# Performance work log

Measured on AMD Instinct MI355X. Metric: run time of the kernel, lower is better.

The kernel has to match this reference:

```python
import jax, jax.numpy as jnp
import numpy as np

W_DIM = 72  # positional_encoding(3 coords, 12 freqs) -> 3*12*2
_F1 = np.array([1.0, 3.0, 3.0, 1.0], dtype=np.float32)
_F2 = np.outer(_F1, _F1); _F2 = _F2 / _F2.sum()  # normalized StyleGAN resample filter


def upsample2x(x):
    """Antialiased 2x upsample: zero-insertion + 4-tap [1,3,3,1] FIR, gain=4 (upfirdn2d)."""
    C = x.shape[1]
    k = jnp.tile(jnp.asarray(_F2 * 4.0, x.dtype)[None, None], (C, 1, 1, 1))  # [C,1,4,4]
    return jax.lax.conv_general_dilated(
        x, k, (1, 1), ((2, 2), (2, 2)), lhs_dilation=(2, 2),
        feature_group_count=C, dimension_numbers=('NCHW', 'OIHW', 'NCHW'))


def affine(w_vec, aw, ab):
    # FullyConnectedLayer: runtime weight gain 1/sqrt(w_dim), bias init 1
    return (w_vec @ aw.T) / np.sqrt(W_DIM) + ab


def mod_conv(x, weight, styles, demodulate=True, padding=1):
    """StyleGAN2 modulated conv2d (batch=1). weight [Co,Ci,k,k], styles [Ci]."""
    w = weight * styles[None, :, None, None]
    if demodulate:
        d = jax.lax.rsqrt(jnp.sum(w * w, axis=(1, 2, 3)) + 1e-8)
        w = w * d[:, None, None, None]
    return jax.lax.conv_general_dilated(
        x, w, (1, 1), ((padding, padding), (padding, padding)),
        dimension_numbers=('NCHW', 'OIHW', 'NCHW'))


def syn_layer(x, w_vec, aw, ab, cw, cb, up):
    s = affine(w_vec, aw, ab)
    if up:
        x = upsample2x(x)
    x = mod_conv(x, cw, s, True, 1)
    # bias_act: lrelu, gain sqrt(2), conv_clamp 256 (noise_strength init 0 -> no noise)
    x = jax.nn.leaky_relu(x + cb[None, :, None, None], 0.2) * np.sqrt(2.0)
    return jnp.clip(x, -256.0, 256.0)


def to_rgb(x, w_vec, aw, ab, cw, cb):
    s = affine(w_vec, aw, ab) / np.sqrt(cw.shape[1])  # ToRGB weight_gain 1/sqrt(Cin)
    y = mod_conv(x, cw, s, False, 0)
    return jnp.clip(y + cb[None, :, None, None], -256.0, 256.0)


def reference(rays, rgbs, conv_w, conv_b, bn_gamma, bn_beta, bn_mean, bn_var,
              a0_w, a0_b, w0, b0, a1_w, a1_b, w1, b1, t0_aw, t0_ab, t0_w, t0_b,
              a2_w, a2_b, w2, b2, a3_w, a3_b, w3, b3, t1_aw, t1_ab, t1_w, t1_b):
    # style vector from positional encoding of ray origin
    p = rays[0, :3, 0, 0]
    fb = 2.0 ** jnp.arange(12, dtype=rays.dtype)
    pts = (p[:, None] * fb[None, :]).reshape(-1)  # (36,)
    w_vec = jnp.concatenate([jnp.sin(pts), jnp.cos(pts)])  # (72,)
    # mapping: 1x1 conv + relu + BatchNorm2d (eval-mode)
    feat = jnp.einsum('oi,bihw->bohw', conv_w[:, :, 0, 0], rgbs) + conv_b[None, :, None, None]
    feat = jax.nn.relu(feat)
    inv = jax.lax.rsqrt(bn_var + 1e-5)
    feat = (feat - bn_mean[None, :, None, None]) * (inv * bn_gamma)[None, :, None, None] + bn_beta[None, :, None, None]
    rgb = feat[:, :3]
    # block0: 32ch@128 -> 256ch@256, skip-architecture ToRGB
    x = syn_layer(feat, w_vec, a0_w, a0_b, w0, b0, True)
    x = syn_layer(x, w_vec, a1_w, a1_b, w1, b1, False)
    img = upsample2x(rgb) + to_rgb(x, w_vec, t0_aw, t0_ab, t0_w, t0_b)
    # block1: 256ch@256 -> 128ch@512
    x = syn_layer(x, w_vec, a2_w, a2_b, w2, b2, True)
    x = syn_layer(x, w_vec, a3_w, a3_b, w3, b3, False)
    img = upsample2x(img) + to_rgb(x, w_vec, t1_aw, t1_ab, t1_w, t1_b)
    return img  # [1,3,512,512]


def setup_inputs() -> dict:
    key = jax.random.key(0)
    ks = jax.random.split(key, 16)
    rn = lambda k, s: jax.random.normal(k, s, dtype=jnp.float32)
    z = lambda s: jnp.zeros(s, jnp.float32)
    o = lambda s: jnp.ones(s, jnp.float32)
    inp = {}
    inp['rays'] = rn(ks[0], (1, 6, 128, 128))
    inp['rgbs'] = jax.random.uniform(ks[1], (1, 3, 128, 128), dtype=jnp.float32)
    inp['conv_w'] = rn(ks[2], (32, 3, 1, 1)); inp['conv_b'] = z((32,))
    inp['bn_gamma'] = o((32,)); inp['bn_beta'] = z((32,))
    inp['bn_mean'] = z((32,)); inp['bn_var'] = o((32,))
    inp['a0_w'] = rn(ks[3], (32, 72)); inp['a0_b'] = o((32,))
    inp['w0'] = rn(ks[4], (256, 32, 3, 3)); inp['b0'] = z((256,))
    inp['a1_w'] = rn(ks[5], (256, 72)); inp['a1_b'] = o((256,))
    inp['w1'] = rn(ks[6], (256, 256, 3, 3)); inp['b1'] = z((256,))
    inp['t0_aw'] = rn(ks[7], (256, 72)); inp['t0_ab'] = o((256,))
    inp['t0_w'] = rn(ks[8], (3, 256, 1, 1)); inp['t0_b'] = z((3,))
    inp['a2_w'] = rn(ks[9], (256, 72)); inp['a2_b'] = o((256,))
    inp['w2'] = rn(ks[10], (128, 256, 3, 3)); inp['b2'] = z((128,))
    inp['a3_w'] = rn(ks[11], (128, 72)); inp['a3_b'] = o((128,))
    inp['w3'] = rn(ks[12], (128, 128, 3, 3)); inp['b3'] = z((128,))
    inp['t1_aw'] = rn(ks[13], (128, 72)); inp['t1_ab'] = o((128,))
    inp['t1_w'] = rn(ks[14], (3, 128, 1, 1)); inp['t1_b'] = z((3,))
    return inp
```

## Files before the change

kernel.cpp:

```cpp
#include <hip/hip_runtime.h>
#include <cstddef>

typedef __attribute__((ext_vector_type(8))) short short8;
typedef __attribute__((ext_vector_type(4))) float f32x4;
typedef __attribute__((address_space(3))) void lds_void;
typedef const __attribute__((address_space(1))) void glob_void;

static const size_t OFF_S0    = 0;
static const size_t OFF_S1    = 64;
static const size_t OFF_S2    = 320;
static const size_t OFF_S3    = 576;
static const size_t OFF_MT0   = 704;
static const size_t OFF_MT1   = 1472;
static const size_t OFF_ZERO  = 1856;
static const size_t OFF_RGBF  = 2048;
static const size_t OFF_IMG0  = 51200;
static const size_t OFF_RGBP  = 247808;
static const size_t OFF_WQ0   = 1900544;
static const size_t OFF_WQ1   = 1937408;
static const size_t OFF_WQ2   = 2232320;
static const size_t OFF_WQ3   = 2379776;
static const size_t OFF_FEAT  = 2453504;
static const size_t OFF_UFEAT = 2715648;
static const size_t OFF_X1    = 4194304;
static const size_t OFF_X2    = 4194304;
static const size_t OFF_U     = 20971520;
static const size_t OFF_X0    = 20971520;

__device__ __forceinline__ unsigned short f2bf(float f) {
  unsigned int u = __float_as_uint(f);
  return (unsigned short)((u + 0x7FFFu + ((u >> 16) & 1u)) >> 16);
}
__device__ __forceinline__ float b2f(short h) {
  return __uint_as_float(((unsigned int)(unsigned short)h) << 16);
}

__global__ void __launch_bounds__(256) prep_kernel(
    const float* __restrict__ rays,
    const float* __restrict__ a0w, const float* __restrict__ a0b,
    const float* __restrict__ a1w, const float* __restrict__ a1b,
    const float* __restrict__ t0aw, const float* __restrict__ t0ab,
    const float* __restrict__ a2w, const float* __restrict__ a2b,
    const float* __restrict__ a3w, const float* __restrict__ a3b,
    const float* __restrict__ t1aw, const float* __restrict__ t1ab,
    const float* __restrict__ t0w, const float* __restrict__ t1w,
    float* __restrict__ ws)
{
  __shared__ float wv[72];
  __shared__ float st0l[256];
  __shared__ float st1l[128];
  const int tid = threadIdx.x;
  if (tid < 128) ws[OFF_ZERO + tid] = 0.f;
  if (tid < 36) {
    int i = tid / 12, j = tid % 12;
    float v = rays[i * 16384] * (float)(1 << j);
    wv[tid]      = sinf(v);
    wv[36 + tid] = cosf(v);
  }
  __syncthreads();
  const float inv72 = 0.11785113019775793f;

  if (tid < 32) {
    float d = 0.f;
    for (int k = 0; k < 72; ++k) d += wv[k] * a0w[tid * 72 + k];
    ws[OFF_S0 + tid] = fmaf(d, inv72, a0b[tid]);
  }
  {
    float d = 0.f;
    for (int k = 0; k < 72; ++k) d += wv[k] * a1w[tid * 72 + k];
    ws[OFF_S1 + tid] = fmaf(d, inv72, a1b[tid]);
  }
  {
    float d = 0.f;
    for (int k = 0; k < 72; ++k) d += wv[k] * t0aw[tid * 72 + k];
    st0l[tid] = fmaf(d, inv72, t0ab[tid]) * 0.0625f;
  }
  {
    float d = 0.f;
    for (int k = 0; k < 72; ++k) d += wv[k] * a2w[tid * 72 + k];
    ws[OFF_S2 + tid] = fmaf(d, inv72, a2b[tid]);
  }
  if (tid < 128) {
    float d = 0.f;
    for (int k = 0; k < 72; ++k) d += wv[k] * a3w[tid * 72 + k];
    ws[OFF_S3 + tid] = fmaf(d, inv72, a3b[tid]);
  }
  if (tid < 128) {
    float d = 0.f;
    for (int k = 0; k < 72; ++k) d += wv[k] * t1aw[tid * 72 + k];
    st1l[tid] = fmaf(d, inv72, t1ab[tid]) * 0.08838834764831845f;
  }
  __syncthreads();
  for (int i = tid; i < 768; i += 256) ws[OFF_MT0 + i] = t0w[i] * st0l[i & 255];
  for (int i = tid; i < 384; i += 256) ws[OFF_MT1 + i] = t1w[i] * st1l[i & 127];
}

__global__ void __launch_bounds__(256) modw_kernel(
    const float* __restrict__ w, const float* __restrict__ s,
    unsigned short* __restrict__ wq, int Ci, int Co)
{
  const int co = blockIdx.x;
  const int n = Ci * 9;
  float local = 0.f;
  for (int i = threadIdx.x; i < n; i += 256) {
    float v = w[co * n + i] * s[i / 9];
    local += v * v;
  }
#pragma unroll
  for (int off = 32; off >= 1; off >>= 1) local += __shfl_xor(local, off);
  __shared__ float red[4];
  if ((threadIdx.x & 63) == 0) red[threadIdx.x >> 6] = local;
  __syncthreads();
  const float d = rsqrtf(red[0] + red[1] + red[2] + red[3] + 1e-8f);
  const int sxor = (co & 3) ^ ((co >> 2) & 3);
  for (int i = threadIdx.x; i < n; i += 256) {
    int ci = i / 9, t = i - ci * 9;
    int kk = ci & 31;
    int sl = (kk >> 3) ^ sxor;
    wq[(((size_t)(ci >> 5) * 9 + t) * Co + co) * 32 + (sl << 3) + (kk & 7)] =
        f2bf(w[co * n + i] * s[ci] * d);
  }
}

__global__ void __launch_bounds__(256) feat_kernel(
    const float* __restrict__ rgbs, const float* __restrict__ cw, const float* __restrict__ cb,
    const float* __restrict__ gam, const float* __restrict__ bet,
    const float* __restrict__ mean, const float* __restrict__ var,
    unsigned short* __restrict__ feat, float* __restrict__ rgbf)
{
  const int p = blockIdx.x * 256 + threadIdx.x;
  const float r = rgbs[p], g = rgbs[16384 + p], b = rgbs[32768 + p];
  unsigned int pk[16];
#pragma unroll
  for (int co = 0; co < 32; ++co) {
    float v = cw[co * 3] * r + cw[co * 3 + 1] * g + cw[co * 3 + 2] * b + cb[co];
    v = fmaxf(v, 0.f);
    float inv = rsqrtf(var[co] + 1e-5f);
    v = (v - mean[co]) * (inv * gam[co]) + bet[co];
    if (co < 3) rgbf[co * 16384 + p] = v;
    unsigned int h = f2bf(v);
    if ((co & 1) == 0) pk[co >> 1] = h;
    else               pk[co >> 1] |= h << 16;
  }
  uint4* dst = reinterpret_cast<uint4*>(feat + (size_t)p * 32);
#pragma unroll
  for (int q = 0; q < 4; ++q)
    dst[q] = make_uint4(pk[q * 4], pk[q * 4 + 1], pk[q * 4 + 2], pk[q * 4 + 3]);
}

__global__ void __launch_bounds__(256) up2x_nhwc_kernel(
    const unsigned short* __restrict__ in, unsigned short* __restrict__ out,
    int H, int W, int c8s , int w2s )
{
  const int cid = blockIdx.x * 256 + threadIdx.x;
  const int k = cid & ((1 << c8s) - 1);
  const int pix = cid >> c8s;
  const int ey = pix >> w2s;
  const int ex = pix & ((1 << w2s) - 1);
  const int C = 8 << c8s;
  int ry0; float ay0, ay1;
  if (ey & 1) { ry0 = ey >> 1;       ay0 = 0.75f; ay1 = 0.25f; }
  else        { ry0 = (ey >> 1) - 1; ay0 = 0.25f; ay1 = 0.75f; }
  int cx0; float bx0, bx1;
  if (ex & 1) { cx0 = ex >> 1;       bx0 = 0.75f; bx1 = 0.25f; }
  else        { cx0 = (ex >> 1) - 1; bx0 = 0.25f; bx1 = 0.75f; }
  const short8 z = {0, 0, 0, 0, 0, 0, 0, 0};
  short8 v00 = z, v01 = z, v10 = z, v11 = z;
  const bool yo0 = (ry0 >= 0), yo1 = (ry0 + 1 < H);
  const bool xo0 = (cx0 >= 0), xo1 = (cx0 + 1 < W);
  if (yo0 && xo0) v00 = *reinterpret_cast<const short8*>(in + ((size_t)(ry0 * W + cx0) * C + k * 8));
  if (yo0 && xo1) v01 = *reinterpret_cast<const short8*>(in + ((size_t)(ry0 * W + cx0 + 1) * C + k * 8));
  if (yo1 && xo0) v10 = *reinterpret_cast<const short8*>(in + ((size_t)((ry0 + 1) * W + cx0) * C + k * 8));
  if (yo1 && xo1) v11 = *reinterpret_cast<const short8*>(in + ((size_t)((ry0 + 1) * W + cx0 + 1) * C + k * 8));
  unsigned int o[4];
#pragma unroll
  for (int j = 0; j < 8; ++j) {
    float f = ay0 * (bx0 * b2f(v00[j]) + bx1 * b2f(v01[j]))
            + ay1 * (bx0 * b2f(v10[j]) + bx1 * b2f(v11[j]));
    unsigned int h = f2bf(f);
    if ((j & 1) == 0) o[j >> 1] = h;
    else              o[j >> 1] |= h << 16;
  }
  *reinterpret_cast<uint4*>(out + (size_t)pix * C + k * 8) = make_uint4(o[0], o[1], o[2], o[3]);
}

template <bool FUSE_RGB>
__global__ void __launch_bounds__(512) conv3x3_mfma(
    const unsigned short* __restrict__ in,
    const unsigned short* __restrict__ wq,
    const float* __restrict__ bias,
    unsigned short* __restrict__ out,
    const float* __restrict__ rgbw,
    float* __restrict__ rgbp,
    const unsigned short* __restrict__ zpage,
    int H, int W, int Ci, int Co)
{
  const int tid  = threadIdx.x;
  const int lane = tid & 63;
  const int wv   = tid >> 6;
  const int wr   = wv & 3;
  const int wg   = wv >> 2;
  const int lo   = lane & 15, hi = lane >> 4;
  const int tpr  = W >> 4;
  const int T_y  = (blockIdx.x / tpr) << 4;
  const int T_x  = (blockIdx.x % tpr) << 4;
  const int cogB = blockIdx.y << 7;
  const int cog  = cogB + (wg << 6);

  __shared__ short8 xs[2][1296];
  __shared__ short8 wlds[2][1536];
  __shared__ float  rw[FUSE_RGB ? 384 : 4];

  if (FUSE_RGB) {
    for (int i = tid; i < 3 * Co; i += 512) rw[i] = rgbw[i];
  }

  f32x4 acc[4][4];
#pragma unroll
  for (int a = 0; a < 4; ++a)
#pragma unroll
    for (int b = 0; b < 4; ++b) acc[a][b] = (f32x4){0.f, 0.f, 0.f, 0.f};

  const unsigned short* gsrc[3];
#pragma unroll
  for (int j = 0; j < 3; ++j) {
    const int s = j * 512 + tid;
    const int pix = s >> 2, kslot = s & 3;
    const int rr = pix / 18, cc = pix - rr * 18;
    const int gy = T_y - 1 + rr, gx = T_x - 1 + cc;
    const int k = kslot ^ ((cc >> 1) & 3);
    const bool inb = (s < 1296) && gy >= 0 && gy < H && gx >= 0 && gx < W;
    gsrc[j] = inb ? (in + ((size_t)(gy * W + gx) * Ci + (k << 3))) : zpage;
  }

#define STAGE(c, buf)                                                              \
  {                                                                                \
    const int cb_ = (c) << 5;                                                      \
    _Pragma("unroll")                                                              \
    for (int j = 0; j < 2; ++j)                                                    \
      __builtin_amdgcn_global_load_lds((glob_void*)(gsrc[j] + cb_),                \
                                       (lds_void*)&xs[buf][j * 512 + tid], 16, 0, 0); \
    if (tid < 272)                                                                 \
      __builtin_amdgcn_global_load_lds((glob_void*)(gsrc[2] + cb_),                \
                                       (lds_void*)&xs[buf][1024 + tid], 16, 0, 0); \
  }

#define STAGE_W(C, KX, BUF)                                                        \
  {                                                                                \
    _Pragma("unroll")                                                              \
    for (int j = 0; j < 3; ++j) {                                                  \
      const unsigned short* src_ =                                                 \
          wq + ((size_t)((C) * 9 + j * 3 + (KX)) * Co + cogB) * 32 + tid * 8;      \
      __builtin_amdgcn_global_load_lds((glob_void*)src_,                           \
                                       (lds_void*)&wlds[BUF][(j << 9) + tid], 16, 0, 0); \
    }                                                                              \
  }

  const int sxa   = (lo & 3) ^ ((lo >> 2) & 3);
  const int wbase = (((wg << 6) + lo) << 2) + (hi ^ sxa);
#define ALOADW(SLOT, KY, BUF)                                                      \
  {                                                                                \
    _Pragma("unroll")                                                              \
    for (int cf = 0; cf < 4; ++cf)                                                 \
      apf[SLOT][cf] = wlds[BUF][((KY) << 9) + wbase + (cf << 6)];                  \
  }

  STAGE(0, 0);
  STAGE_W(0, 0, 0);
  __syncthreads();

  const int nch = Ci >> 5;
  const int rstride = 72;
  int wb = 0;
  for (int c = 0; c < nch; ++c) {
    const int cur = c & 1;
#pragma unroll
    for (int g = 0; g < 3; ++g) {
      if (g < 2)             { STAGE_W(c, g + 1, wb ^ 1); }
      else if (c + 1 < nch)  { STAGE_W(c + 1, 0, wb ^ 1); }
      if (g == 0 && c + 1 < nch) STAGE(c + 1, cur ^ 1);

      const int tx2  = lo + g;
      const int xv_  = hi ^ ((tx2 >> 1) & 3);
      const int rowb = (((wr << 2) * 18 + tx2) << 2) + xv_;
      short8 b0 = xs[cur][rowb];
      short8 b1 = xs[cur][rowb + rstride];
      short8 b2 = xs[cur][rowb + 2 * rstride];
      short8 b3 = xs[cur][rowb + 3 * rstride];

      short8 apf[2][4];
      ALOADW(0, 0, wb);
      ALOADW(1, 1, wb);
#pragma unroll
      for (int cf = 0; cf < 4; ++cf) {
        acc[cf][0] = __builtin_amdgcn_mfma_f32_16x16x32_bf16(apf[0][cf], b0, acc[cf][0], 0, 0, 0);
        acc[cf][1] = __builtin_amdgcn_mfma_f32_16x16x32_bf16(apf[0][cf], b1, acc[cf][1], 0, 0, 0);
        acc[cf][2] = __builtin_amdgcn_mfma_f32_16x16x32_bf16(apf[0][cf], b2, acc[cf][2], 0, 0, 0);
        acc[cf][3] = __builtin_amdgcn_mfma_f32_16x16x32_bf16(apf[0][cf], b3, acc[cf][3], 0, 0, 0);
      }
      b0 = xs[cur][rowb + 4 * rstride];
      ALOADW(0, 2, wb);
#pragma unroll
      for (int cf = 0; cf < 4; ++cf) {
        acc[cf][0] = __builtin_amdgcn_mfma_f32_16x16x32_bf16(apf[1][cf], b1, acc[cf][0], 0, 0, 0);
        acc[cf][1] = __builtin_amdgcn_mfma_f32_16x16x32_bf16(apf[1][cf], b2, acc[cf][1], 0, 0, 0);
        acc[cf][2] = __builtin_amdgcn_mfma_f32_16x16x32_bf16(apf[1][cf], b3, acc[cf][2], 0, 0, 0);
        acc[cf][3] = __builtin_amdgcn_mfma_f32_16x16x32_bf16(apf[1][cf], b0, acc[cf][3], 0, 0, 0);
      }
      b1 = xs[cur][rowb + 5 * rstride];
#pragma unroll
      for (int cf = 0; cf < 4; ++cf) {
        acc[cf][0] = __builtin_amdgcn_mfma_f32_16x16x32_bf16(apf[0][cf], b2, acc[cf][0], 0, 0, 0);
        acc[cf][1] = __builtin_amdgcn_mfma_f32_16x16x32_bf16(apf[0][cf], b3, acc[cf][1], 0, 0, 0);
        acc[cf][2] = __builtin_amdgcn_mfma_f32_16x16x32_bf16(apf[0][cf], b0, acc[cf][2], 0, 0, 0);
        acc[cf][3] = __builtin_amdgcn_mfma_f32_16x16x32_bf16(apf[0][cf], b1, acc[cf][3], 0, 0, 0);
      }
      __syncthreads();
      wb ^= 1;
    }
  }
#undef STAGE
#undef STAGE_W
#undef ALOADW

  const float rt2 = 1.41421356237309515f;
#pragma unroll
  for (int r = 0; r < 4; ++r) {
    const int gy = T_y + (wr << 2) + r;
    const int gx = T_x + lo;
    if (!FUSE_RGB) {
#pragma unroll
      for (int cf = 0; cf < 4; ++cf) {
        const int cb = cog + (cf << 4) + (hi << 2);
        const f32x4 bi = *reinterpret_cast<const f32x4*>(bias + cb);
        unsigned short h[4];
#pragma unroll
        for (int reg = 0; reg < 4; ++reg) {
          float vv = acc[cf][r][reg] + bi[reg];
          vv = (vv >= 0.f) ? vv : 0.2f * vv;
          vv *= rt2;
          vv = fminf(fmaxf(vv, -256.f), 256.f);
          h[reg] = f2bf(vv);
        }
        uint2 pk;
        pk.x = (unsigned int)h[0] | ((unsigned int)h[1] << 16);
        pk.y = (unsigned int)h[2] | ((unsigned int)h[3] << 16);
        *reinterpret_cast<uint2*>(out + (size_t)(gy * W + gx) * Co + cb) = pk;
      }
    } else {
      float p0 = 0.f, p1 = 0.f, p2 = 0.f;
#pragma unroll
      for (int cf = 0; cf < 4; ++cf) {
        const int cb = cog + (cf << 4) + (hi << 2);
        const f32x4 bi = *reinterpret_cast<const f32x4*>(bias + cb);
#pragma unroll
        for (int reg = 0; reg < 4; ++reg) {
          float vv = acc[cf][r][reg] + bi[reg];
          vv = (vv >= 0.f) ? vv : 0.2f * vv;
          vv *= rt2;
          vv = fminf(fmaxf(vv, -256.f), 256.f);
          p0 = fmaf(rw[cb + reg], vv, p0);
          p1 = fmaf(rw[Co + cb + reg], vv, p1);
          p2 = fmaf(rw[2 * Co + cb + reg], vv, p2);
        }
      }
      p0 += __shfl_xor(p0, 16); p0 += __shfl_xor(p0, 32);
      p1 += __shfl_xor(p1, 16); p1 += __shfl_xor(p1, 32);
      p2 += __shfl_xor(p2, 16); p2 += __shfl_xor(p2, 32);
      if (hi == 0) {
        const size_t HWs = (size_t)H * W;
        const size_t px  = (size_t)gy * W + gx;
        rgbp[((size_t)wg * 3 + 0) * HWs + px] = p0;
        rgbp[((size_t)wg * 3 + 1) * HWs + px] = p1;
        rgbp[((size_t)wg * 3 + 2) * HWs + px] = p2;
      }
    }
  }
}

__device__ __forceinline__ float up2x_sample(const float* __restrict__ im, int H, int W,
                                             int oy, int ox)
{
  int my = oy >> 1, mx = ox >> 1;
  int ry0; float ay0, ay1;
  if (oy & 1) { ry0 = my;     ay0 = 0.75f; ay1 = 0.25f; }
  else        { ry0 = my - 1; ay0 = 0.25f; ay1 = 0.75f; }
  int cx0; float bx0, bx1;
  if (ox & 1) { cx0 = mx;     bx0 = 0.75f; bx1 = 0.25f; }
  else        { cx0 = mx - 1; bx0 = 0.25f; bx1 = 0.75f; }
  float v00 = (ry0 >= 0    && cx0 >= 0   ) ? im[ry0 * W + cx0]           : 0.f;
  float v01 = (ry0 >= 0    && cx0 + 1 < W) ? im[ry0 * W + cx0 + 1]       : 0.f;
  float v10 = (ry0 + 1 < H && cx0 >= 0   ) ? im[(ry0 + 1) * W + cx0]     : 0.f;
  float v11 = (ry0 + 1 < H && cx0 + 1 < W) ? im[(ry0 + 1) * W + cx0 + 1] : 0.f;
  return ay0 * (bx0 * v00 + bx1 * v01) + ay1 * (bx0 * v10 + bx1 * v11);
}

__global__ void __launch_bounds__(256) img0_kernel(
    const float* __restrict__ rgbf, const unsigned short* __restrict__ x1,
    const float* __restrict__ mt0g, const float* __restrict__ tb,
    float* __restrict__ img0)
{
  __shared__ float mt[768];
  const int tid = threadIdx.x;
  for (int i = tid; i < 768; i += 256) mt[i] = mt0g[i];
  __syncthreads();
  const int p = blockIdx.x * 256 + tid;
  const unsigned short* xp = x1 + (size_t)p * 256;
  float a0 = 0.f, a1 = 0.f, a2 = 0.f;
  for (int i8 = 0; i8 < 32; ++i8) {
    const short8 v = *reinterpret_cast<const short8*>(xp + i8 * 8);
#pragma unroll
    for (int j = 0; j < 8; ++j) {
      const float xv = b2f(v[j]);
      const int ci = i8 * 8 + j;
      a0 = fmaf(mt[ci],       xv, a0);
      a1 = fmaf(mt[256 + ci], xv, a1);
      a2 = fmaf(mt[512 + ci], xv, a2);
    }
  }
  const int oy = p >> 8, ox = p & 255;
  float av[3] = {a0, a1, a2};
#pragma unroll
  for (int o = 0; o < 3; ++o) {
    float y = fminf(fmaxf(av[o] + tb[o], -256.f), 256.f);
    img0[o * 65536 + p] = up2x_sample(rgbf + o * 16384, 128, 128, oy, ox) + y;
  }
}

__global__ void __launch_bounds__(256) final_kernel(
    const float* __restrict__ img0, const float* __restrict__ rgbp,
    const float* __restrict__ tb, float* __restrict__ out)
{
  const int p = blockIdx.x * 256 + threadIdx.x;
  const int oy = p >> 9, ox = p & 511;
#pragma unroll
  for (int o = 0; o < 3; ++o) {
    float a = rgbp[(0 * 3 + o) * 262144 + p] + rgbp[(1 * 3 + o) * 262144 + p];
    float y = fminf(fmaxf(a + tb[o], -256.f), 256.f);
    out[o * 262144 + p] = up2x_sample(img0 + o * 65536, 256, 256, oy, ox) + y;
  }
}

extern "C" void kernel_launch(void* const* d_in, const int* in_sizes, int n_in,
                              void* d_out, int out_size, void* d_ws, size_t ws_size,
                              hipStream_t stream)
{
  const float* rays   = (const float*)d_in[0];
  const float* rgbs   = (const float*)d_in[1];
  const float* conv_w = (const float*)d_in[2];
  const float* conv_b = (const float*)d_in[3];
  const float* bn_g   = (const float*)d_in[4];
  const float* bn_b   = (const float*)d_in[5];
  const float* bn_m   = (const float*)d_in[6];
  const float* bn_v   = (const float*)d_in[7];
  const float* a0_w   = (const float*)d_in[8];
  const float* a0_b   = (const float*)d_in[9];
  const float* w0     = (const float*)d_in[10];
  const float* b0     = (const float*)d_in[11];
  const float* a1_w   = (const float*)d_in[12];
  const float* a1_b   = (const float*)d_in[13];
  const float* w1     = (const float*)d_in[14];
  const float* b1     = (const float*)d_in[15];
  const float* t0_aw  = (const float*)d_in[16];
  const float* t0_ab  = (const float*)d_in[17];
  const float* t0_w   = (const float*)d_in[18];
  const float* t0_b   = (const float*)d_in[19];
  const float* a2_w   = (const float*)d_in[20];
  const float* a2_b   = (const float*)d_in[21];
  const float* w2     = (const float*)d_in[22];
  const float* b2     = (const float*)d_in[23];
  const float* a3_w   = (const float*)d_in[24];
  const float* a3_b   = (const float*)d_in[25];
  const float* w3     = (const float*)d_in[26];
  const float* b3     = (const float*)d_in[27];
  const float* t1_aw  = (const float*)d_in[28];
  const float* t1_ab  = (const float*)d_in[29];
  const float* t1_w   = (const float*)d_in[30];
  const float* t1_b   = (const float*)d_in[31];

  float* ws  = (float*)d_ws;
  float* out = (float*)d_out;

  unsigned short* wq0   = (unsigned short*)(ws + OFF_WQ0);
  unsigned short* wq1   = (unsigned short*)(ws + OFF_WQ1);
  unsigned short* wq2   = (unsigned short*)(ws + OFF_WQ2);
  unsigned short* wq3   = (unsigned short*)(ws + OFF_WQ3);
  unsigned short* featb = (unsigned short*)(ws + OFF_FEAT);
  unsigned short* ufeat = (unsigned short*)(ws + OFF_UFEAT);
  unsigned short* x0b   = (unsigned short*)(ws + OFF_X0);
  unsigned short* x1b   = (unsigned short*)(ws + OFF_X1);
  unsigned short* x2b   = (unsigned short*)(ws + OFF_X2);
  unsigned short* Ub    = (unsigned short*)(ws + OFF_U);
  const unsigned short* zpage = (const unsigned short*)(ws + OFF_ZERO);

  prep_kernel<<<1, 256, 0, stream>>>(rays, a0_w, a0_b, a1_w, a1_b, t0_aw, t0_ab,
                                     a2_w, a2_b, a3_w, a3_b, t1_aw, t1_ab,
                                     t0_w, t1_w, ws);
  modw_kernel<<<256, 256, 0, stream>>>(w0, ws + OFF_S0, wq0, 32, 256);
  modw_kernel<<<256, 256, 0, stream>>>(w1, ws + OFF_S1, wq1, 256, 256);
  modw_kernel<<<128, 256, 0, stream>>>(w2, ws + OFF_S2, wq2, 256, 128);
  modw_kernel<<<128, 256, 0, stream>>>(w3, ws + OFF_S3, wq3, 128, 128);
  feat_kernel<<<64, 256, 0, stream>>>(rgbs, conv_w, conv_b, bn_g, bn_b, bn_m, bn_v,
                                      featb, ws + OFF_RGBF);
  up2x_nhwc_kernel<<<1024, 256, 0, stream>>>(featb, ufeat, 128, 128, 2, 8);
  conv3x3_mfma<false><<<dim3(256, 2), 512, 0, stream>>>(
      ufeat, wq0, b0, x0b, nullptr, nullptr, zpage, 256, 256, 32, 256);
  conv3x3_mfma<false><<<dim3(256, 2), 512, 0, stream>>>(
      x0b, wq1, b1, x1b, nullptr, nullptr, zpage, 256, 256, 256, 256);
  img0_kernel<<<256, 256, 0, stream>>>(ws + OFF_RGBF, x1b, ws + OFF_MT0, t0_b,
                                       ws + OFF_IMG0);
  up2x_nhwc_kernel<<<32768, 256, 0, stream>>>(x1b, Ub, 256, 256, 5, 9);
  conv3x3_mfma<false><<<dim3(1024, 1), 512, 0, stream>>>(
      Ub, wq2, b2, x2b, nullptr, nullptr, zpage, 512, 512, 256, 128);
  conv3x3_mfma<true><<<dim3(1024, 1), 512, 0, stream>>>(
      x2b, wq3, b3, nullptr, ws + OFF_MT1, ws + OFF_RGBP, zpage, 512, 512, 128, 128);
  final_kernel<<<1024, 256, 0, stream>>>(ws + OFF_IMG0, ws + OFF_RGBP, t1_b, out);
}
```

Before: 463.4 us.

## Double conv tile height to 32 rows per block for weight reuse

Each conv block now computes a 32x16 pixel tile instead of 16x16, with each wave handling 8 output rows. The staged input halo grows to 34x18 and the accumulator count doubles. Each weight fragment loaded from LDS now feeds twice as many MFMAs, and there is less halo overhead per output pixel. In exchange the grid shrinks by half, so fewer blocks fill the GPU, and LDS use and register pressure rise, which may lower occupancy.

```diff
diff --git a/kernel.cpp b/kernel.cpp
--- a/kernel.cpp
+++ b/kernel.cpp
@@ -202,12 +202,12 @@
   const int wg   = wv >> 2;
   const int lo   = lane & 15, hi = lane >> 4;
   const int tpr  = W >> 4;
-  const int T_y  = (blockIdx.x / tpr) << 4;
+  const int T_y  = (blockIdx.x / tpr) << 5;
   const int T_x  = (blockIdx.x % tpr) << 4;
   const int cogB = blockIdx.y << 7;
   const int cog  = cogB + (wg << 6);
 
-  __shared__ short8 xs[2][1296];
+  __shared__ short8 xs[2][2448];
   __shared__ short8 wlds[2][1536];
   __shared__ float  rw[FUSE_RGB ? 384 : 4];
 
@@ -215,21 +215,21 @@
     for (int i = tid; i < 3 * Co; i += 512) rw[i] = rgbw[i];
   }
 
-  f32x4 acc[4][4];
+  f32x4 acc[4][8];
 #pragma unroll
   for (int a = 0; a < 4; ++a)
 #pragma unroll
-    for (int b = 0; b < 4; ++b) acc[a][b] = (f32x4){0.f, 0.f, 0.f, 0.f};
-
-  const unsigned short* gsrc[3];
-#pragma unroll
-  for (int j = 0; j < 3; ++j) {
+    for (int b = 0; b < 8; ++b) acc[a][b] = (f32x4){0.f, 0.f, 0.f, 0.f};
+
+  const unsigned short* gsrc[5];
+#pragma unroll
+  for (int j = 0; j < 5; ++j) {
     const int s = j * 512 + tid;
     const int pix = s >> 2, kslot = s & 3;
     const int rr = pix / 18, cc = pix - rr * 18;
     const int gy = T_y - 1 + rr, gx = T_x - 1 + cc;
     const int k = kslot ^ ((cc >> 1) & 3);
-    const bool inb = (s < 1296) && gy >= 0 && gy < H && gx >= 0 && gx < W;
+    const bool inb = (s < 2448) && gy >= 0 && gy < H && gx >= 0 && gx < W;
     gsrc[j] = inb ? (in + ((size_t)(gy * W + gx) * Ci + (k << 3))) : zpage;
   }
 
@@ -237,12 +237,12 @@
   {                                                                                \
     const int cb_ = (c) << 5;                                                      \
     _Pragma("unroll")                                                              \
-    for (int j = 0; j < 2; ++j)                                                    \
+    for (int j = 0; j < 4; ++j)                                                    \
       __builtin_amdgcn_global_load_lds((glob_void*)(gsrc[j] + cb_),                \
                                        (lds_void*)&xs[buf][j * 512 + tid], 16, 0, 0); \
-    if (tid < 272)                                                                 \
-      __builtin_amdgcn_global_load_lds((glob_void*)(gsrc[2] + cb_),                \
-                                       (lds_void*)&xs[buf][1024 + tid], 16, 0, 0); \
+    if (tid < 400)                                                                 \
+      __builtin_amdgcn_global_load_lds((glob_void*)(gsrc[4] + cb_),                \
+                                       (lds_void*)&xs[buf][2048 + tid], 16, 0, 0); \
   }
 
 #define STAGE_W(C, KX, BUF)                                                        \
@@ -265,6 +265,8 @@
       apf[SLOT][cf] = wlds[BUF][((KY) << 9) + wbase + (cf << 6)];                  \
   }
 
+#define MF(A, B, C) __builtin_amdgcn_mfma_f32_16x16x32_bf16(A, B, C, 0, 0, 0)
+
   STAGE(0, 0);
   STAGE_W(0, 0, 0);
   __syncthreads();
@@ -282,38 +284,55 @@
 
       const int tx2  = lo + g;
       const int xv_  = hi ^ ((tx2 >> 1) & 3);
-      const int rowb = (((wr << 2) * 18 + tx2) << 2) + xv_;
-      short8 b0 = xs[cur][rowb];
-      short8 b1 = xs[cur][rowb + rstride];
-      short8 b2 = xs[cur][rowb + 2 * rstride];
-      short8 b3 = xs[cur][rowb + 3 * rstride];
+      const int rowb = (((wr << 3) * 18 + tx2) << 2) + xv_;
+
+      short8 q0 = xs[cur][rowb];
+      short8 q1 = xs[cur][rowb + rstride];
+      short8 q2 = xs[cur][rowb + 2 * rstride];
+      short8 q3 = xs[cur][rowb + 3 * rstride];
+      short8 q4 = xs[cur][rowb + 4 * rstride];
+      short8 q5 = xs[cur][rowb + 5 * rstride];
+      short8 q6 = xs[cur][rowb + 6 * rstride];
+      short8 q7 = xs[cur][rowb + 7 * rstride];
 
       short8 apf[2][4];
       ALOADW(0, 0, wb);
       ALOADW(1, 1, wb);
 #pragma unroll
       for (int cf = 0; cf < 4; ++cf) {
-        acc[cf][0] = __builtin_amdgcn_mfma_f32_16x16x32_bf16(apf[0][cf], b0, acc[cf][0], 0, 0, 0);
-        acc[cf][1] = __builtin_amdgcn_mfma_f32_16x16x32_bf16(apf[0][cf], b1, acc[cf][1], 0, 0, 0);
-        acc[cf][2] = __builtin_amdgcn_mfma_f32_16x16x32_bf16(apf[0][cf], b2, acc[cf][2], 0, 0, 0);
-        acc[cf][3] = __builtin_amdgcn_mfma_f32_16x16x32_bf16(apf[0][cf], b3, acc[cf][3], 0, 0, 0);
+        acc[cf][0] = MF(apf[0][cf], q0, acc[cf][0]);
+        acc[cf][1] = MF(apf[0][cf], q1, acc[cf][1]);
+        acc[cf][2] = MF(apf[0][cf], q2, acc[cf][2]);
+        acc[cf][3] = MF(apf[0][cf], q3, acc[cf][3]);
+        acc[cf][4] = MF(apf[0][cf], q4, acc[cf][4]);
+        acc[cf][5] = MF(apf[0][cf], q5, acc[cf][5]);
+        acc[cf][6] = MF(apf[0][cf], q6, acc[cf][6]);
+        acc[cf][7] = MF(apf[0][cf], q7, acc[cf][7]);
       }
-      b0 = xs[cur][rowb + 4 * rstride];
+      short8 q8 = xs[cur][rowb + 8 * rstride];
       ALOADW(0, 2, wb);
 #pragma unroll
       for (int cf = 0; cf < 4; ++cf) {
-        acc[cf][0] = __builtin_amdgcn_mfma_f32_16x16x32_bf16(apf[1][cf], b1, acc[cf][0], 0, 0, 0);
-        acc[cf][1] = __builtin_amdgcn_mfma_f32_16x16x32_bf16(apf[1][cf], b2, acc[cf][1], 0, 0, 0);
-        acc[cf][2] = __builtin_amdgcn_mfma_f32_16x16x32_bf16(apf[1][cf], b3, acc[cf][2], 0, 0, 0);
-        acc[cf][3] = __builtin_amdgcn_mfma_f32_16x16x32_bf16(apf[1][cf], b0, acc[cf][3], 0, 0, 0);
+        acc[cf][0] = MF(apf[1][cf], q1, acc[cf][0]);
+        acc[cf][1] = MF(apf[1][cf], q2, acc[cf][1]);
+        acc[cf][2] = MF(apf[1][cf], q3, acc[cf][2]);
+        acc[cf][3] = MF(apf[1][cf], q4, acc[cf][3]);
+        acc[cf][4] = MF(apf[1][cf], q5, acc[cf][4]);
+        acc[cf][5] = MF(apf[1][cf], q6, acc[cf][5]);
+        acc[cf][6] = MF(apf[1][cf], q7, acc[cf][6]);
+        acc[cf][7] = MF(apf[1][cf], q8, acc[cf][7]);
       }
-      b1 = xs[cur][rowb + 5 * rstride];
+      short8 q9 = xs[cur][rowb + 9 * rstride];
 #pragma unroll
       for (int cf = 0; cf < 4; ++cf) {
-        acc[cf][0] = __builtin_amdgcn_mfma_f32_16x16x32_bf16(apf[0][cf], b2, acc[cf][0], 0, 0, 0);
-        acc[cf][1] = __builtin_amdgcn_mfma_f32_16x16x32_bf16(apf[0][cf], b3, acc[cf][1], 0, 0, 0);
-        acc[cf][2] = __builtin_amdgcn_mfma_f32_16x16x32_bf16(apf[0][cf], b0, acc[cf][2], 0, 0, 0);
-        acc[cf][3] = __builtin_amdgcn_mfma_f32_16x16x32_bf16(apf[0][cf], b1, acc[cf][3], 0, 0, 0);
+        acc[cf][0] = MF(apf[0][cf], q2, acc[cf][0]);
+        acc[cf][1] = MF(apf[0][cf], q3, acc[cf][1]);
+        acc[cf][2] = MF(apf[0][cf], q4, acc[cf][2]);
+        acc[cf][3] = MF(apf[0][cf], q5, acc[cf][3]);
+        acc[cf][4] = MF(apf[0][cf], q6, acc[cf][4]);
+        acc[cf][5] = MF(apf[0][cf], q7, acc[cf][5]);
+        acc[cf][6] = MF(apf[0][cf], q8, acc[cf][6]);
+        acc[cf][7] = MF(apf[0][cf], q9, acc[cf][7]);
       }
       __syncthreads();
       wb ^= 1;
@@ -322,11 +341,12 @@
 #undef STAGE
 #undef STAGE_W
 #undef ALOADW
+#undef MF
 
   const float rt2 = 1.41421356237309515f;
 #pragma unroll
-  for (int r = 0; r < 4; ++r) {
-    const int gy = T_y + (wr << 2) + r;
+  for (int r = 0; r < 8; ++r) {
+    const int gy = T_y + (wr << 3) + r;
     const int gx = T_x + lo;
     if (!FUSE_RGB) {
 #pragma unroll
@@ -503,16 +523,16 @@
   feat_kernel<<<64, 256, 0, stream>>>(rgbs, conv_w, conv_b, bn_g, bn_b, bn_m, bn_v,
                                       featb, ws + OFF_RGBF);
   up2x_nhwc_kernel<<<1024, 256, 0, stream>>>(featb, ufeat, 128, 128, 2, 8);
-  conv3x3_mfma<false><<<dim3(256, 2), 512, 0, stream>>>(
+  conv3x3_mfma<false><<<dim3(128, 2), 512, 0, stream>>>(
       ufeat, wq0, b0, x0b, nullptr, nullptr, zpage, 256, 256, 32, 256);
-  conv3x3_mfma<false><<<dim3(256, 2), 512, 0, stream>>>(
+  conv3x3_mfma<false><<<dim3(128, 2), 512, 0, stream>>>(
       x0b, wq1, b1, x1b, nullptr, nullptr, zpage, 256, 256, 256, 256);
   img0_kernel<<<256, 256, 0, stream>>>(ws + OFF_RGBF, x1b, ws + OFF_MT0, t0_b,
                                        ws + OFF_IMG0);
   up2x_nhwc_kernel<<<32768, 256, 0, stream>>>(x1b, Ub, 256, 256, 5, 9);
-  conv3x3_mfma<false><<<dim3(1024, 1), 512, 0, stream>>>(
+  conv3x3_mfma<false><<<dim3(512, 1), 512, 0, stream>>>(
       Ub, wq2, b2, x2b, nullptr, nullptr, zpage, 512, 512, 256, 128);
-  conv3x3_mfma<true><<<dim3(1024, 1), 512, 0, stream>>>(
+  conv3x3_mfma<true><<<dim3(512, 1), 512, 0, stream>>>(
       x2b, wq3, b3, nullptr, ws + OFF_MT1, ws + OFF_RGBP, zpage, 512, 512, 128, 128);
   final_kernel<<<1024, 256, 0, stream>>>(ws + OFF_IMG0, ws + OFF_RGBP, t1_b, out);
 }
```

Measured after the change: 409.5 us. 11.6% less time.
